# Kernel optimization log

Hardware: AMD Instinct MI355X
Metric: run time of the kernel (lower is better)

## Reference

```python
import jax, jax.numpy as jnp
import numpy as np

EPS = 1e-12
K_APPNP = 3
ALPHA = 0.5

def setup_inputs() -> dict:
    key = jax.random.key(0)
    kg, kz, k1, k2, k3 = jax.random.split(key, 5)
    N, out_dim, hid_dim = 10000, 128, 256
    g = jax.random.uniform(kg, (N, N), dtype=jnp.float32)
    z = jax.random.normal(kz, (N, out_dim), dtype=jnp.float32)
    def xavier(k, shape):
        fan_out, fan_in = shape
        lim = float(np.sqrt(6.0 / (fan_in + fan_out)))
        return jax.random.uniform(k, shape, jnp.float32, -lim, lim)
    # torch Linear weight is [out_features, in_features]
    W1 = xavier(k1, (hid_dim, out_dim))    # res1: out_dim -> hid_dim
    W1_ = xavier(k2, (hid_dim, hid_dim))   # res1_: hid -> hid
    W2 = xavier(k3, (out_dim, hid_dim))    # res2: hid -> out_dim
    return {"g": g, "z": z, "W1": W1, "W1_": W1_, "W2": W2}

def _graph_conv(g, x, W, act):
    # dropout is identity in eval mode
    return act((g @ x) @ W.T)

def _appnp(g, H):
    Z = H
    for _ in range(K_APPNP):
        Z = (1.0 - ALPHA) * (g @ Z) + ALPHA * H
    return Z

def reference(g, z, W1, W1_, W2):
    z1 = _graph_conv(g, z, W1, jax.nn.relu)       # [N, hid]
    z_ = _graph_conv(g, z1, W1_, jax.nn.relu)     # [N, hid]
    # torch.tensor(z_) detaches from the autograd graph
    zn = jax.lax.stop_gradient(z_)
    norm = jnp.maximum(jnp.linalg.norm(zn, axis=1, keepdims=True), EPS)
    zn = zn / norm                                 # F.normalize(p=2, dim=1)
    Z = _appnp(g, zn)                              # [N, hid]
    res = _graph_conv(g, z_, W2, jax.nn.sigmoid)   # [N, out]
    return (res, Z)
```

## Files before the change

### kernel.cpp

```cpp
#include <hip/hip_runtime.h>
#include <stdint.h>

typedef __attribute__((ext_vector_type(8))) short short8;
typedef __attribute__((ext_vector_type(4))) float f32x4;
typedef __attribute__((ext_vector_type(4))) unsigned short us4;

#define MFMA16(a,b,c) __builtin_amdgcn_mfma_f32_16x16x32_bf16((a),(b),(c),0,0,0)

static __device__ __forceinline__ float bf2f(unsigned short u){
  union { float f; unsigned int i; } c; c.i = ((unsigned int)u) << 16; return c.f;
}
static __device__ __forceinline__ unsigned short f2bf(float f){
  union { float f; unsigned int i; } c; c.f = f;
  unsigned int x = c.i;
  unsigned int r = x + 0x7fffu + ((x >> 16) & 1u);
  return (unsigned short)(r >> 16);
}

typedef const __attribute__((address_space(1))) void cg_void;
typedef __attribute__((address_space(3))) void lds_void;
static __device__ __forceinline__ void gl_lds16(const void* g, void* l){
  __builtin_amdgcn_global_load_lds((cg_void*)g, (lds_void*)l, 16, 0, 0);
}

#define MROWS 10240LL

__global__ void k_conv_g(const float* __restrict__ g, unsigned short* __restrict__ o){
  const int CH = 2512;
  const long long total = 10240LL * CH;
  for (long long i = (long long)blockIdx.x*blockDim.x + threadIdx.x; i < total;
       i += (long long)gridDim.x*blockDim.x){
    int r = (int)(i / CH);
    int c4 = (int)(i % CH) * 4;
    us4 v = {0,0,0,0};
    if (r < 10000 && c4 < 10000){
      float4 f = *(const float4*)(g + (long long)r*10000 + c4);
      v.x = f2bf(f.x); v.y = f2bf(f.y); v.z = f2bf(f.z); v.w = f2bf(f.w);
    }
    *(us4*)(o + (long long)r*10048 + c4) = v;
  }
}

__global__ void k_conv(const float* __restrict__ in, unsigned short* __restrict__ o, int n4){
  for (int i = blockIdx.x*blockDim.x + threadIdx.x; i < n4; i += gridDim.x*blockDim.x){
    float4 f = *(const float4*)(in + (long long)i*4);
    us4 v; v.x=f2bf(f.x); v.y=f2bf(f.y); v.z=f2bf(f.z); v.w=f2bf(f.w);
    *(us4*)(o + (long long)i*4) = v;
  }
}

__global__ void k_tconv_z(const float* __restrict__ z, unsigned short* __restrict__ o){
  __shared__ unsigned short t[64][65];
  const int rb = blockIdx.x*64, cb = blockIdx.y*64;
  #pragma unroll
  for (int it = 0; it < 4; ++it){
    int idx = it*256 + threadIdx.x;
    int r = idx >> 4, c4 = (idx & 15) * 4;
    float4 f = {0.f,0.f,0.f,0.f};
    if (rb + r < 10000) f = *(const float4*)(z + (long long)(rb+r)*128 + cb + c4);
    t[c4+0][r] = f2bf(f.x); t[c4+1][r] = f2bf(f.y);
    t[c4+2][r] = f2bf(f.z); t[c4+3][r] = f2bf(f.w);
  }
  __syncthreads();
  #pragma unroll
  for (int it = 0; it < 4; ++it){
    int idx = it*256 + threadIdx.x;
    int ro = idx >> 4, co4 = (idx & 15) * 4;
    us4 v; v.x=t[ro][co4]; v.y=t[ro][co4+1]; v.z=t[ro][co4+2]; v.w=t[ro][co4+3];
    *(us4*)(o + (long long)(cb+ro)*10048 + rb + co4) = v;
  }
}

__global__ void k_t_bf16(const unsigned short* __restrict__ in, unsigned short* __restrict__ o){
  __shared__ unsigned short t[64][65];
  const int rb = blockIdx.x*64, cb = blockIdx.y*64;
  #pragma unroll
  for (int it = 0; it < 4; ++it){
    int idx = it*256 + threadIdx.x;
    int r = idx >> 4, c4 = (idx & 15) * 4;
    us4 v = {0,0,0,0};
    if (rb + r < 10000) v = *(const us4*)(in + (long long)(rb+r)*256 + cb + c4);
    t[c4+0][r]=v.x; t[c4+1][r]=v.y; t[c4+2][r]=v.z; t[c4+3][r]=v.w;
  }
  __syncthreads();
  #pragma unroll
  for (int it = 0; it < 4; ++it){
    int idx = it*256 + threadIdx.x;
    int ro = idx >> 4, co4 = (idx & 15)*4;
    us4 v; v.x=t[ro][co4]; v.y=t[ro][co4+1]; v.z=t[ro][co4+2]; v.w=t[ro][co4+3];
    *(us4*)(o + (long long)(cb+ro)*10048 + rb + co4) = v;
  }
}

__global__ void k_rownorm(const unsigned short* __restrict__ in, unsigned short* __restrict__ o){
  const int w = threadIdx.x >> 6, l = threadIdx.x & 63;
  const int row = blockIdx.x*4 + w;
  us4 v = *(const us4*)(in + (long long)row*256 + l*4);
  float a = bf2f(v.x), b = bf2f(v.y), c = bf2f(v.z), d = bf2f(v.w);
  float ss = a*a + b*b + c*c + d*d;
  #pragma unroll
  for (int off = 32; off; off >>= 1) ss += __shfl_xor(ss, off, 64);
  float s = 1.0f / fmaxf(sqrtf(ss), 1e-12f);
  us4 r; r.x=f2bf(a*s); r.y=f2bf(b*s); r.z=f2bf(c*s); r.w=f2bf(d*s);
  *(us4*)(o + (long long)row*256 + l*4) = r;
}

__global__ __launch_bounds__(512)
void k_gemm8(const unsigned short* __restrict__ A,
             const unsigned short* __restrict__ B,
             float* __restrict__ P, int S, int ldp)
{
  constexpr int LDA = 10048;
  __shared__ unsigned short sm[2][32768];

  const int tid = threadIdx.x;
  const int wid = tid >> 6, l = tid & 63;
  const int wm = wid >> 2, wn = wid & 3;
  const int lr = l & 15, lk = l >> 4;
  const int mBase = blockIdx.x * 256;
  const int nBase = blockIdx.y * 256;
  const int s = blockIdx.z;
  const int kt0 = (157 * s) / S, kt1 = (157 * (s + 1)) / S;

  auto stage_half = [&](unsigned short* dst, int kt, int h){
    const unsigned short* base = (h < 2) ? A : B;
    const int rowBase = ((h < 2) ? mBase : nBase) + (h & 1) * 128;
    const int ldsOff = ((h < 2) ? 0 : 16384) + (h & 1) * 8192;
    #pragma unroll
    for (int i = 0; i < 2; ++i){
      int ch = tid + 512 * i;
      int row = ch >> 3, gc = (ch & 7) ^ (row & 7);
      gl_lds16(base + (long long)(rowBase + row) * LDA + kt * 64 + gc * 8,
               dst + ldsOff + ch * 8);
    }
  };

  f32x4 acc[8][4];
  #pragma unroll
  for (int i = 0; i < 8; ++i)
    #pragma unroll
    for (int j = 0; j < 4; ++j){ f32x4 zz = {0.f,0.f,0.f,0.f}; acc[i][j] = zz; }

  {
    unsigned short* d0 = &sm[0][0];
    stage_half(d0, kt0, 0); stage_half(d0, kt0, 1);
    stage_half(d0, kt0, 2); stage_half(d0, kt0, 3);
  }

  int cur = 0;
  for (int kt = kt0; kt < kt1; ++kt){
    const bool pf = (kt + 1 < kt1);
    unsigned short* nb = &sm[cur ^ 1][0];
    const unsigned short* sp = &sm[cur][0];
    #pragma unroll
    for (int q = 0; q < 4; ++q){
      const int ih = q >> 1, jh = q & 1;
      if (q == 0){
        if (pf) stage_half(nb, kt + 1, 0);
        __builtin_amdgcn_sched_barrier(0);
        if (pf) asm volatile("s_waitcnt vmcnt(2)" ::: "memory");
        else    asm volatile("s_waitcnt vmcnt(0)" ::: "memory");
        __builtin_amdgcn_sched_barrier(0);
        __builtin_amdgcn_s_barrier();
        __builtin_amdgcn_sched_barrier(0);
      }
      short8 af[4][2], bf[2][2];
      #pragma unroll
      for (int ii = 0; ii < 4; ++ii){
        const int row = wm*128 + (ih*4 + ii)*16 + lr;
        #pragma unroll
        for (int ks = 0; ks < 2; ++ks)
          af[ii][ks] = *(const short8*)(sp + row*64 + (((ks*4 + lk) ^ (row & 7)) * 8));
      }
      #pragma unroll
      for (int jj = 0; jj < 2; ++jj){
        const int row = wn*64 + (jh*2 + jj)*16 + lr;
        #pragma unroll
        for (int ks = 0; ks < 2; ++ks)
          bf[jj][ks] = *(const short8*)(sp + 16384 + row*64 + (((ks*4 + lk) ^ (row & 7)) * 8));
      }
      if (q != 0){
        if (pf) stage_half(nb, kt + 1, q);
        __builtin_amdgcn_sched_barrier(0);
        __builtin_amdgcn_s_barrier();
        __builtin_amdgcn_sched_barrier(0);
      }
      __builtin_amdgcn_s_setprio(1);
      #pragma unroll
      for (int ks = 0; ks < 2; ++ks)
        #pragma unroll
        for (int ii = 0; ii < 4; ++ii)
          #pragma unroll
          for (int jj = 0; jj < 2; ++jj)
            acc[ih*4+ii][jh*2+jj] =
              MFMA16(af[ii][ks], bf[jj][ks], acc[ih*4+ii][jh*2+jj]);
      __builtin_amdgcn_s_setprio(0);
      __builtin_amdgcn_sched_barrier(0);
      __builtin_amdgcn_s_barrier();
      __builtin_amdgcn_sched_barrier(0);
    }
    cur ^= 1;
  }

  float* Pp = P + (long long)s * MROWS * ldp;
  #pragma unroll
  for (int i = 0; i < 8; ++i){
    const int row0 = mBase + wm*128 + i*16 + lk*4;
    #pragma unroll
    for (int j = 0; j < 4; ++j){
      const int col = nBase + wn*64 + j*16 + lr;
      #pragma unroll
      for (int r = 0; r < 4; ++r)
        Pp[(long long)(row0 + r)*ldp + col] = acc[i][j][r];
    }
  }
}

template<int BN, int NWM, int NWN>
__global__ __launch_bounds__(256)
void k_gemm(const unsigned short* __restrict__ A,
            const unsigned short* __restrict__ B,
            float* __restrict__ P, int S, int ldp)
{
  constexpr int LDA = 10048;
  constexpr int BM  = 64;
  constexpr int WM = BM / NWM, WN = BN / NWN;
  constexpr int MF = WM / 16, NF = WN / 16;
  constexpr int AE = BM * 64;
  constexpr int BE = BN * 64;
  constexpr int ACH = BM * 8 / 256;
  constexpr int BCH = BN * 8 / 256;

  __shared__ unsigned short sm[2][AE + BE];

  const int tid = threadIdx.x, w = tid >> 6, l = tid & 63;
  const int lr = l & 15, lk = l >> 4, swz = l & 7;
  const int wm = w / NWN, wn = w % NWN;
  const int mBase = blockIdx.x * BM;
  const int nBase = blockIdx.y * BN;
  const int s = blockIdx.z;
  const int kt0 = (157 * s) / S, kt1 = (157 * (s + 1)) / S;

  auto stage = [&](int buf, int kt){
    unsigned short* dst = &sm[buf][0];
    const unsigned short* Ak = A + (long long)kt * 64;
    const unsigned short* Bk = B + (long long)kt * 64;
    #pragma unroll
    for (int i = 0; i < ACH; ++i){
      int c = i * 256 + tid;
      int row = c >> 3, gr = c & 7;
      gl_lds16(Ak + (long long)(mBase + row) * LDA + ((gr ^ (row & 7)) * 8),
               dst + c * 8);
    }
    #pragma unroll
    for (int i = 0; i < BCH; ++i){
      int c = i * 256 + tid;
      int row = c >> 3, gr = c & 7;
      gl_lds16(Bk + (long long)(nBase + row) * LDA + ((gr ^ (row & 7)) * 8),
               dst + AE + c * 8);
    }
  };

  f32x4 acc[MF][NF];
  #pragma unroll
  for (int i = 0; i < MF; ++i)
    #pragma unroll
    for (int j = 0; j < NF; ++j){ f32x4 zz = {0.f,0.f,0.f,0.f}; acc[i][j] = zz; }

  stage(0, kt0);
  int cur = 0;
  for (int kt = kt0; kt < kt1; ++kt){
    __syncthreads();
    if (kt + 1 < kt1) stage(cur ^ 1, kt + 1);
    const unsigned short* sp = &sm[cur][0];
    #pragma unroll
    for (int ks = 0; ks < 2; ++ks){
      short8 a[MF], b[NF];
      #pragma unroll
      for (int i = 0; i < MF; ++i){
        int row = wm * WM + i * 16 + lr;
        a[i] = *(const short8*)(sp + row * 64 + (((4*ks + lk) ^ swz) * 8));
      }
      #pragma unroll
      for (int j = 0; j < NF; ++j){
        int row = wn * WN + j * 16 + lr;
        b[j] = *(const short8*)(sp + AE + row * 64 + (((4*ks + lk) ^ swz) * 8));
      }
      #pragma unroll
      for (int i = 0; i < MF; ++i)
        #pragma unroll
        for (int j = 0; j < NF; ++j)
          acc[i][j] = MFMA16(a[i], b[j], acc[i][j]);
    }
    cur ^= 1;
  }

  float* Pp = P + (long long)s * MROWS * ldp;
  #pragma unroll
  for (int i = 0; i < MF; ++i){
    const int row0 = mBase + wm * WM + i * 16 + lk * 4;
    #pragma unroll
    for (int j = 0; j < NF; ++j){
      const int col = nBase + wn * WN + j * 16 + lr;
      #pragma unroll
      for (int r = 0; r < 4; ++r)
        Pp[(long long)(row0 + r) * ldp + col] = acc[i][j][r];
    }
  }
}

template<int EPI>
__global__ void k_reduce(const float* __restrict__ P, int S, int ldp, int colOff,
                         int lg, void* __restrict__ out, int ldc,
                         const unsigned short* __restrict__ H)
{
  const long long stride = MROWS * ldp;
  const int idx = blockIdx.x * 256 + threadIdx.x;
  const int row = idx >> lg;
  const int c4 = (idx & ((1 << lg) - 1)) * 4;
  const float* p = P + (long long)row * ldp + colOff + c4;
  float4 sv = *(const float4*)p;
  for (int s2 = 1; s2 < S; ++s2){
    float4 t = *(const float4*)(p + (long long)s2 * stride);
    sv.x += t.x; sv.y += t.y; sv.z += t.z; sv.w += t.w;
  }
  if constexpr (EPI >= 1){
    us4 h = *(const us4*)(H + (long long)row * 256 + c4);
    sv.x = 0.5f*sv.x + 0.5f*bf2f(h.x);
    sv.y = 0.5f*sv.y + 0.5f*bf2f(h.y);
    sv.z = 0.5f*sv.z + 0.5f*bf2f(h.z);
    sv.w = 0.5f*sv.w + 0.5f*bf2f(h.w);
  }
  if constexpr (EPI == 2){
    *(float4*)((float*)out + (long long)row * ldc + c4) = sv;
  } else {
    us4 o; o.x=f2bf(sv.x); o.y=f2bf(sv.y); o.z=f2bf(sv.z); o.w=f2bf(sv.w);
    *(us4*)((unsigned short*)out + (long long)row * ldc + c4) = o;
  }
}

template<int NW, int KW, int ACT>
__global__ __launch_bounds__(320)
void k_gemm_small(const unsigned short* __restrict__ A,
                  const unsigned short* __restrict__ W,
                  void* __restrict__ out)
{
  const int tid = threadIdx.x, w = tid >> 6, l = tid & 63;
  const int lr = l & 15, lk = l >> 4;
  const int mBase = blockIdx.x * 80;
  constexpr int NF = NW/16;

  f32x4 acc[NF];
  #pragma unroll
  for (int f = 0; f < NF; ++f){ f32x4 zz = {0.f,0.f,0.f,0.f}; acc[f] = zz; }

  const unsigned short* ap = A + (long long)(mBase + 16*w + lr)*KW + lk*8;
  #pragma unroll
  for (int kc = 0; kc < KW/32; ++kc){
    short8 a = *(const short8*)(ap + kc*32);
    #pragma unroll
    for (int f = 0; f < NF; ++f){
      short8 b = *(const short8*)(W + (long long)(16*f + lr)*KW + kc*32 + lk*8);
      acc[f] = MFMA16(a, b, acc[f]);
    }
  }

  const int row0 = mBase + 16*w + lk*4;
  #pragma unroll
  for (int f = 0; f < NF; ++f){
    const int col = 16*f + lr;
    #pragma unroll
    for (int r = 0; r < 4; ++r){
      const long long idx = (long long)(row0 + r)*NW + col;
      float v = acc[f][r];
      if constexpr (ACT == 0) ((unsigned short*)out)[idx] = f2bf(fmaxf(v, 0.0f));
      else                    ((float*)out)[idx] = 1.0f / (1.0f + expf(-v));
    }
  }
}

extern "C" void kernel_launch(void* const* d_in, const int* in_sizes, int n_in,
                              void* d_out, int out_size, void* d_ws, size_t ws_size,
                              hipStream_t stream)
{
  const float* g   = (const float*)d_in[0];
  const float* z   = (const float*)d_in[1];
  const float* W1  = (const float*)d_in[2];
  const float* W1_ = (const float*)d_in[3];
  const float* W2  = (const float*)d_in[4];

  char* ws = (char*)d_ws;
  size_t off = 0;
  auto alloc = [&](size_t bytes)->void*{
    void* p = ws + off; off += (bytes + 255) & ~(size_t)255; return p;
  };
  unsigned short* g16  = (unsigned short*)alloc(10240ULL*10048*2);
  unsigned short* zT   = (unsigned short*)alloc(128ULL*10048*2);
  unsigned short* W1c  = (unsigned short*)alloc(256ULL*128*2);
  unsigned short* W1_c = (unsigned short*)alloc(256ULL*256*2);
  unsigned short* W2c  = (unsigned short*)alloc(128ULL*256*2);
  unsigned short* tbuf = (unsigned short*)alloc(10000ULL*256*2);
  unsigned short* Xbuf = (unsigned short*)alloc(10000ULL*256*2);
  unsigned short* Tbuf = (unsigned short*)alloc(512ULL*10048*2);
  unsigned short* zn   = (unsigned short*)alloc(10000ULL*256*2);
  float*          P    = (float*)alloc(10240ULL*1536*4);
  (void)ws_size; (void)in_sizes; (void)n_in; (void)out_size;

  float* res  = (float*)d_out;
  float* Zout = (float*)d_out + 10000LL*128;

  k_conv_g<<<dim3(2048), dim3(256), 0, stream>>>(g, g16);
  k_tconv_z<<<dim3(157,2), dim3(256), 0, stream>>>(z, zT);
  k_conv<<<dim3(32), dim3(256), 0, stream>>>(W1,  W1c,  256*128/4);
  k_conv<<<dim3(64), dim3(256), 0, stream>>>(W1_, W1_c, 256*256/4);
  k_conv<<<dim3(32), dim3(256), 0, stream>>>(W2,  W2c,  128*256/4);

  k_gemm<128,2,2><<<dim3(157,1,3), dim3(256), 0, stream>>>(g16, zT, P, 3, 128);
  k_reduce<0><<<dim3(1250), dim3(256), 0, stream>>>(P, 3, 128, 0, 5, tbuf, 128, nullptr);
  k_gemm_small<256,128,0><<<dim3(125), dim3(320), 0, stream>>>(tbuf, W1c, Xbuf);
  k_t_bf16<<<dim3(157,4), dim3(256), 0, stream>>>(Xbuf, Tbuf);
  k_gemm8<<<dim3(40,1,6), dim3(512), 0, stream>>>(g16, Tbuf, P, 6, 256);
  k_reduce<0><<<dim3(2500), dim3(256), 0, stream>>>(P, 6, 256, 0, 6, tbuf, 256, nullptr);
  k_gemm_small<256,256,0><<<dim3(125), dim3(320), 0, stream>>>(tbuf, W1_c, Xbuf);
  k_rownorm<<<dim3(2500), dim3(256), 0, stream>>>(Xbuf, zn);
  k_t_bf16<<<dim3(157,4), dim3(256), 0, stream>>>(Xbuf, Tbuf);
  k_t_bf16<<<dim3(157,4), dim3(256), 0, stream>>>(zn, Tbuf + 256LL*10048);
  k_gemm8<<<dim3(40,2,3), dim3(512), 0, stream>>>(g16, Tbuf, P, 3, 512);
  k_reduce<0><<<dim3(2500), dim3(256), 0, stream>>>(P, 3, 512, 0,   6, tbuf, 256, nullptr);
  k_reduce<1><<<dim3(2500), dim3(256), 0, stream>>>(P, 3, 512, 256, 6, Xbuf, 256, zn);
  k_gemm_small<128,256,1><<<dim3(125), dim3(320), 0, stream>>>(tbuf, W2c, res);
  k_t_bf16<<<dim3(157,4), dim3(256), 0, stream>>>(Xbuf, Tbuf);
  k_gemm8<<<dim3(40,1,6), dim3(512), 0, stream>>>(g16, Tbuf, P, 6, 256);
  k_reduce<1><<<dim3(2500), dim3(256), 0, stream>>>(P, 6, 256, 0, 6, Xbuf, 256, zn);
  k_t_bf16<<<dim3(157,4), dim3(256), 0, stream>>>(Xbuf, Tbuf);
  k_gemm8<<<dim3(40,1,6), dim3(512), 0, stream>>>(g16, Tbuf, P, 6, 256);
  k_reduce<2><<<dim3(2500), dim3(256), 0, stream>>>(P, 6, 256, 0, 6, Zout, 256, zn);
}
```

Baseline: 648.6 us.

## Fuse rownorm, reduce+transpose, and weight conversions; restructure gemm8 prefetch

Merges the three weight-conversion launches into one kernel. The row L2 normalisation moves into the epilogue of the small GEMM, and the APPNP reduce step is fused with the bf16 transpose into a new reduce_T kernel. Together these remove several launches and intermediate round-trips through global memory. The big GEMM now precomputes its staging addresses and issues the whole next-tile prefetch at the top of each k-step with a single barrier, instead of spreading quarter loads between compute phases, which reduces barriers but may lose some load/compute interleaving.

Result: slower. 667.3 us (+2.9%).

```diff
diff --git a/kernel.cpp b/kernel.cpp
--- a/kernel.cpp
+++ b/kernel.cpp
@@ -41,11 +41,18 @@
   }
 }
 
-__global__ void k_conv(const float* __restrict__ in, unsigned short* __restrict__ o, int n4){
-  for (int i = blockIdx.x*blockDim.x + threadIdx.x; i < n4; i += gridDim.x*blockDim.x){
-    float4 f = *(const float4*)(in + (long long)i*4);
+__global__ void k_conv_w(const float* __restrict__ a, unsigned short* __restrict__ oa, int na4,
+                         const float* __restrict__ b, unsigned short* __restrict__ ob, int nb4,
+                         const float* __restrict__ c, unsigned short* __restrict__ oc, int nc4){
+  for (int i = blockIdx.x*blockDim.x + threadIdx.x; i < na4 + nb4 + nc4;
+       i += gridDim.x*blockDim.x){
+    const float* src; unsigned short* dst; int j = i;
+    if (j < na4){ src = a; dst = oa; }
+    else if (j < na4 + nb4){ j -= na4; src = b; dst = ob; }
+    else { j -= na4 + nb4; src = c; dst = oc; }
+    float4 f = *(const float4*)(src + (long long)j*4);
     us4 v; v.x=f2bf(f.x); v.y=f2bf(f.y); v.z=f2bf(f.z); v.w=f2bf(f.w);
-    *(us4*)(o + (long long)i*4) = v;
+    *(us4*)(dst + (long long)j*4) = v;
   }
 }
 
@@ -90,19 +97,6 @@
     us4 v; v.x=t[ro][co4]; v.y=t[ro][co4+1]; v.z=t[ro][co4+2]; v.w=t[ro][co4+3];
     *(us4*)(o + (long long)(cb+ro)*10048 + rb + co4) = v;
   }
-}
-
-__global__ void k_rownorm(const unsigned short* __restrict__ in, unsigned short* __restrict__ o){
-  const int w = threadIdx.x >> 6, l = threadIdx.x & 63;
-  const int row = blockIdx.x*4 + w;
-  us4 v = *(const us4*)(in + (long long)row*256 + l*4);
-  float a = bf2f(v.x), b = bf2f(v.y), c = bf2f(v.z), d = bf2f(v.w);
-  float ss = a*a + b*b + c*c + d*d;
-  #pragma unroll
-  for (int off = 32; off; off >>= 1) ss += __shfl_xor(ss, off, 64);
-  float s = 1.0f / fmaxf(sqrtf(ss), 1e-12f);
-  us4 r; r.x=f2bf(a*s); r.y=f2bf(b*s); r.z=f2bf(c*s); r.w=f2bf(d*s);
-  *(us4*)(o + (long long)row*256 + l*4) = r;
 }
 
 __global__ __launch_bounds__(512)
@@ -122,7 +116,10 @@
   const int s = blockIdx.z;
   const int kt0 = (157 * s) / S, kt1 = (157 * (s + 1)) / S;
 
-  auto stage_half = [&](unsigned short* dst, int kt, int h){
+  const unsigned short* gsrc[8];
+  int ldst[8];
+  #pragma unroll
+  for (int h = 0; h < 4; ++h){
     const unsigned short* base = (h < 2) ? A : B;
     const int rowBase = ((h < 2) ? mBase : nBase) + (h & 1) * 128;
     const int ldsOff = ((h < 2) ? 0 : 16384) + (h & 1) * 8192;
@@ -130,9 +127,15 @@
     for (int i = 0; i < 2; ++i){
       int ch = tid + 512 * i;
       int row = ch >> 3, gc = (ch & 7) ^ (row & 7);
-      gl_lds16(base + (long long)(rowBase + row) * LDA + kt * 64 + gc * 8,
-               dst + ldsOff + ch * 8);
-    }
+      gsrc[h*2+i] = base + (long long)(rowBase + row) * LDA + gc * 8;
+      ldst[h*2+i] = ldsOff + ch * 8;
+    }
+  }
+  auto stage_tile = [&](unsigned short* dst, int kt){
+    const long long ko = (long long)kt * 64;
+    #pragma unroll
+    for (int i = 0; i < 8; ++i)
+      gl_lds16(gsrc[i] + ko, dst + ldst[i]);
   };
 
   f32x4 acc[8][4];
@@ -141,29 +144,28 @@
     #pragma unroll
     for (int j = 0; j < 4; ++j){ f32x4 zz = {0.f,0.f,0.f,0.f}; acc[i][j] = zz; }
 
-  {
-    unsigned short* d0 = &sm[0][0];
-    stage_half(d0, kt0, 0); stage_half(d0, kt0, 1);
-    stage_half(d0, kt0, 2); stage_half(d0, kt0, 3);
-  }
+  stage_tile(&sm[0][0], kt0);
 
   int cur = 0;
   for (int kt = kt0; kt < kt1; ++kt){
     const bool pf = (kt + 1 < kt1);
     unsigned short* nb = &sm[cur ^ 1][0];
     const unsigned short* sp = &sm[cur][0];
+
+    if (pf){
+      stage_tile(nb, kt + 1);
+      __builtin_amdgcn_sched_barrier(0);
+      asm volatile("s_waitcnt vmcnt(8)" ::: "memory");
+    } else {
+      asm volatile("s_waitcnt vmcnt(0)" ::: "memory");
+    }
+    __builtin_amdgcn_sched_barrier(0);
+    __builtin_amdgcn_s_barrier();
+    __builtin_amdgcn_sched_barrier(0);
+
     #pragma unroll
     for (int q = 0; q < 4; ++q){
       const int ih = q >> 1, jh = q & 1;
-      if (q == 0){
-        if (pf) stage_half(nb, kt + 1, 0);
-        __builtin_amdgcn_sched_barrier(0);
-        if (pf) asm volatile("s_waitcnt vmcnt(2)" ::: "memory");
-        else    asm volatile("s_waitcnt vmcnt(0)" ::: "memory");
-        __builtin_amdgcn_sched_barrier(0);
-        __builtin_amdgcn_s_barrier();
-        __builtin_amdgcn_sched_barrier(0);
-      }
       short8 af[4][2], bf[2][2];
       #pragma unroll
       for (int ii = 0; ii < 4; ++ii){
@@ -178,12 +180,6 @@
         #pragma unroll
         for (int ks = 0; ks < 2; ++ks)
           bf[jj][ks] = *(const short8*)(sp + 16384 + row*64 + (((ks*4 + lk) ^ (row & 7)) * 8));
-      }
-      if (q != 0){
-        if (pf) stage_half(nb, kt + 1, q);
-        __builtin_amdgcn_sched_barrier(0);
-        __builtin_amdgcn_s_barrier();
-        __builtin_amdgcn_sched_barrier(0);
       }
       __builtin_amdgcn_s_setprio(1);
       #pragma unroll
@@ -324,14 +320,12 @@
     float4 t = *(const float4*)(p + (long long)s2 * stride);
     sv.x += t.x; sv.y += t.y; sv.z += t.z; sv.w += t.w;
   }
-  if constexpr (EPI >= 1){
+  if constexpr (EPI == 2){
     us4 h = *(const us4*)(H + (long long)row * 256 + c4);
     sv.x = 0.5f*sv.x + 0.5f*bf2f(h.x);
     sv.y = 0.5f*sv.y + 0.5f*bf2f(h.y);
     sv.z = 0.5f*sv.z + 0.5f*bf2f(h.z);
     sv.w = 0.5f*sv.w + 0.5f*bf2f(h.w);
-  }
-  if constexpr (EPI == 2){
     *(float4*)((float*)out + (long long)row * ldc + c4) = sv;
   } else {
     us4 o; o.x=f2bf(sv.x); o.y=f2bf(sv.y); o.z=f2bf(sv.z); o.w=f2bf(sv.w);
@@ -339,11 +333,50 @@
   }
 }
 
-template<int NW, int KW, int ACT>
+__global__ void k_reduce_T(const float* __restrict__ P, int S, int ldp, int colOff,
+                           unsigned short* __restrict__ outT,
+                           const unsigned short* __restrict__ H)
+{
+  __shared__ unsigned short t[64][65];
+  const int rb = blockIdx.x*64, cb = blockIdx.y*64;
+  const long long stride = MROWS * (long long)ldp;
+  #pragma unroll
+  for (int it = 0; it < 4; ++it){
+    int idx = it*256 + threadIdx.x;
+    int r = idx >> 4, c4 = (idx & 15)*4;
+    int row = rb + r;
+    float4 sv = {0.f,0.f,0.f,0.f};
+    if (row < 10000){
+      const float* p = P + (long long)row*ldp + colOff + cb + c4;
+      sv = *(const float4*)p;
+      for (int s2 = 1; s2 < S; ++s2){
+        float4 tt = *(const float4*)(p + (long long)s2*stride);
+        sv.x += tt.x; sv.y += tt.y; sv.z += tt.z; sv.w += tt.w;
+      }
+      us4 h = *(const us4*)(H + (long long)row*256 + cb + c4);
+      sv.x = 0.5f*sv.x + 0.5f*bf2f(h.x);
+      sv.y = 0.5f*sv.y + 0.5f*bf2f(h.y);
+      sv.z = 0.5f*sv.z + 0.5f*bf2f(h.z);
+      sv.w = 0.5f*sv.w + 0.5f*bf2f(h.w);
+    }
+    t[c4+0][r] = f2bf(sv.x); t[c4+1][r] = f2bf(sv.y);
+    t[c4+2][r] = f2bf(sv.z); t[c4+3][r] = f2bf(sv.w);
+  }
+  __syncthreads();
+  #pragma unroll
+  for (int it = 0; it < 4; ++it){
+    int idx = it*256 + threadIdx.x;
+    int ro = idx >> 4, co4 = (idx & 15)*4;
+    us4 v; v.x=t[ro][co4]; v.y=t[ro][co4+1]; v.z=t[ro][co4+2]; v.w=t[ro][co4+3];
+    *(us4*)(outT + (long long)(cb+ro)*10048 + rb + co4) = v;
+  }
+}
+
+template<int NW, int KW, int ACT, int DONORM>
 __global__ __launch_bounds__(320)
 void k_gemm_small(const unsigned short* __restrict__ A,
                   const unsigned short* __restrict__ W,
-                  void* __restrict__ out)
+                  void* __restrict__ out, unsigned short* __restrict__ out2)
 {
   const int tid = threadIdx.x, w = tid >> 6, l = tid & 63;
   const int lr = l & 15, lk = l >> 4;
@@ -366,15 +399,44 @@
   }
 
   const int row0 = mBase + 16*w + lk*4;
-  #pragma unroll
-  for (int f = 0; f < NF; ++f){
-    const int col = 16*f + lr;
+  if constexpr (DONORM){
+    float ss[4] = {0.f,0.f,0.f,0.f};
+    #pragma unroll
+    for (int f = 0; f < NF; ++f)
+      #pragma unroll
+      for (int r = 0; r < 4; ++r){
+        float v = fmaxf(acc[f][r], 0.0f);
+        acc[f][r] = v;
+        ss[r] += v*v;
+      }
     #pragma unroll
     for (int r = 0; r < 4; ++r){
-      const long long idx = (long long)(row0 + r)*NW + col;
-      float v = acc[f][r];
-      if constexpr (ACT == 0) ((unsigned short*)out)[idx] = f2bf(fmaxf(v, 0.0f));
-      else                    ((float*)out)[idx] = 1.0f / (1.0f + expf(-v));
+      #pragma unroll
+      for (int off = 1; off <= 8; off <<= 1)
+        ss[r] += __shfl_xor(ss[r], off, 64);
+      ss[r] = 1.0f / fmaxf(sqrtf(ss[r]), 1e-12f);
+    }
+    #pragma unroll
+    for (int f = 0; f < NF; ++f){
+      const int col = 16*f + lr;
+      #pragma unroll
+      for (int r = 0; r < 4; ++r){
+        const long long idx = (long long)(row0 + r)*NW + col;
+        ((unsigned short*)out)[idx] = f2bf(acc[f][r]);
+        out2[idx] = f2bf(acc[f][r] * ss[r]);
+      }
+    }
+  } else {
+    #pragma unroll
+    for (int f = 0; f < NF; ++f){
+      const int col = 16*f + lr;
+      #pragma unroll
+      for (int r = 0; r < 4; ++r){
+        const long long idx = (long long)(row0 + r)*NW + col;
+        float v = acc[f][r];
+        if constexpr (ACT == 0) ((unsigned short*)out)[idx] = f2bf(fmaxf(v, 0.0f));
+        else                    ((float*)out)[idx] = 1.0f / (1.0f + expf(-v));
+      }
     }
   }
 }
@@ -411,28 +473,25 @@
 
   k_conv_g<<<dim3(2048), dim3(256), 0, stream>>>(g, g16);
   k_tconv_z<<<dim3(157,2), dim3(256), 0, stream>>>(z, zT);
-  k_conv<<<dim3(32), dim3(256), 0, stream>>>(W1,  W1c,  256*128/4);
-  k_conv<<<dim3(64), dim3(256), 0, stream>>>(W1_, W1_c, 256*256/4);
-  k_conv<<<dim3(32), dim3(256), 0, stream>>>(W2,  W2c,  128*256/4);
+  k_conv_w<<<dim3(120), dim3(256), 0, stream>>>(W1, W1c, 256*128/4,
+                                                W1_, W1_c, 256*256/4,
+                                                W2, W2c, 128*256/4);
 
   k_gemm<128,2,2><<<dim3(157,1,3), dim3(256), 0, stream>>>(g16, zT, P, 3, 128);
   k_reduce<0><<<dim3(1250), dim3(256), 0, stream>>>(P, 3, 128, 0, 5, tbuf, 128, nullptr);
-  k_gemm_small<256,128,0><<<dim3(125), dim3(320), 0, stream>>>(tbuf, W1c, Xbuf);
+  k_gemm_small<256,128,0,0><<<dim3(125), dim3(320), 0, stream>>>(tbuf, W1c, Xbuf, nullptr);
   k_t_bf16<<<dim3(157,4), dim3(256), 0, stream>>>(Xbuf, Tbuf);
   k_gemm8<<<dim3(40,1,6), dim3(512), 0, stream>>>(g16, Tbuf, P, 6, 256);
   k_reduce<0><<<dim3(2500), dim3(256), 0, stream>>>(P, 6, 256, 0, 6, tbuf, 256, nullptr);
-  k_gemm_small<256,256,0><<<dim3(125), dim3(320), 0, stream>>>(tbuf, W1_c, Xbuf);
-  k_rownorm<<<dim3(2500), dim3(256), 0, stream>>>(Xbuf, zn);
+  k_gemm_small<256,256,0,1><<<dim3(125), dim3(320), 0, stream>>>(tbuf, W1_c, Xbuf, zn);
   k_t_bf16<<<dim3(157,4), dim3(256), 0, stream>>>(Xbuf, Tbuf);
   k_t_bf16<<<dim3(157,4), dim3(256), 0, stream>>>(zn, Tbuf + 256LL*10048);
   k_gemm8<<<dim3(40,2,3), dim3(512), 0, stream>>>(g16, Tbuf, P, 3, 512);
-  k_reduce<0><<<dim3(2500), dim3(256), 0, stream>>>(P, 3, 512, 0,   6, tbuf, 256, nullptr);
-  k_reduce<1><<<dim3(2500), dim3(256), 0, stream>>>(P, 3, 512, 256, 6, Xbuf, 256, zn);
-  k_gemm_small<128,256,1><<<dim3(125), dim3(320), 0, stream>>>(tbuf, W2c, res);
-  k_t_bf16<<<dim3(157,4), dim3(256), 0, stream>>>(Xbuf, Tbuf);
+  k_reduce<0><<<dim3(2500), dim3(256), 0, stream>>>(P, 3, 512, 0, 6, tbuf, 256, nullptr);
+  k_reduce_T<<<dim3(157,4), dim3(256), 0, stream>>>(P, 3, 512, 256, Tbuf, zn);
+  k_gemm_small<128,256,1,0><<<dim3(125), dim3(320), 0, stream>>>(tbuf, W2c, res, nullptr);
   k_gemm8<<<dim3(40,1,6), dim3(512), 0, stream>>>(g16, Tbuf, P, 6, 256);
-  k_reduce<1><<<dim3(2500), dim3(256), 0, stream>>>(P, 6, 256, 0, 6, Xbuf, 256, zn);
-  k_t_bf16<<<dim3(157,4), dim3(256), 0, stream>>>(Xbuf, Tbuf);
+  k_reduce_T<<<dim3(157,4), dim3(256), 0, stream>>>(P, 6, 256, 0, Tbuf, zn);
   k_gemm8<<<dim3(40,1,6), dim3(512), 0, stream>>>(g16, Tbuf, P, 6, 256);
   k_reduce<2><<<dim3(2500), dim3(256), 0, stream>>>(P, 6, 256, 0, 6, Zout, 256, zn);
 }
```
